# Optimization experiments

Hardware: AMD Instinct MI355X
Metric: run time of the kernel (lower is better)

Reference implementation:

```python
import jax, jax.numpy as jnp
import numpy as np

CLIPS_NUM = 4
OUTPUT_SIZE = 1000000  # outputSize: number of features in trainset (scales Z)
T = 0.07               # temperature
QUEUE_K = 131072       # queue size
D = 128                # inputSize (feature dim)
BS = 256               # batch_size * clips_num


def _l2norm(x):
    return x / jnp.linalg.norm(x, axis=-1, keepdims=True)


def setup_inputs() -> dict:
    key = jax.random.key(0)
    kq, kk, km = jax.random.split(key, 3)
    # MoCo-style L2-normalized features keep exp(sim/T) finite.
    q = _l2norm(jax.random.normal(kq, (BS, D), jnp.float32))
    k = _l2norm(jax.random.normal(kk, (BS, D), jnp.float32))
    memory = _l2norm(jax.random.normal(km, (QUEUE_K, D), jnp.float32))
    return {"q": q, "k": k, "memory": memory, "i": 0}


def _make_indices(bs, clips_num):
    """Static (numpy) replication of MemoryMoCo.prepare_indices."""
    batch_size = bs // clips_num
    # indices[v] = row indices of all clips of video v: [batch_size, clips_num]
    indices = np.arange(bs).reshape(clips_num, batch_size).T
    vid = np.arange(bs) % batch_size
    all_clips = vid[:, None] + np.arange(clips_num)[None, :] * batch_size  # [bs, clips_num]
    mask = all_clips != np.arange(bs)[:, None]
    pos_indices = all_clips[mask].reshape(bs, clips_num - 1)  # drop self
    return jnp.asarray(indices), jnp.asarray(pos_indices)


def reference(q, k, memory, i):
    bs, d = q.shape
    batch_size = bs // CLIPS_NUM
    indices, pos_indices = _make_indices(bs, CLIPS_NUM)

    k = jax.lax.stop_gradient(k)            # k = k.detach()
    mem = jax.lax.stop_gradient(memory)     # queue = memory.clone().detach()

    # l_pos: gather positives, per-row bmm with q, mean over positives -> [bs, 1]
    positives = k[pos_indices]              # [bs, clips_num-1, d]
    l_pos = jnp.mean(jnp.einsum('bpd,bd->bp', positives, q), axis=-1, keepdims=True)

    # l_neg: queue GEMM -> [bs, K]
    l_neg = q @ mem.T

    out = jnp.concatenate([l_pos, l_neg], axis=1)   # [bs, 1+K]
    out = jnp.exp(out / T)
    # First-call NCE normalization: Z = out.mean() * outputSize (Z is detached in torch)
    Z = jax.lax.stop_gradient(jnp.mean(out) * OUTPUT_SIZE)
    out = out / Z

    probs = jnp.mean(out[:, 0] / jnp.sum(out, axis=1))  # extract_probs

    # no_grad memory-bank update: scatter mean of each video's clip keys
    out_ids = jnp.arange(batch_size) % memory.shape[0]   # index=0, fmod queueSize
    k_mean = jnp.mean(k[indices], axis=1)                # [batch_size, d]
    new_memory = memory.at[out_ids].set(k_mean)

    return out, probs, new_memory
```

## Files before the change

### kernel.cpp

```cpp
#include <hip/hip_runtime.h>
#include <hip/hip_bf16.h>

constexpr int       DIM        = 128;
constexpr long long CN         = 131073;
constexpr long long OUT_ELEMS  = 256LL * 131073LL;
constexpr long long PROBS_OFF  = OUT_ELEMS;
constexpr long long MEMOUT_OFF = OUT_ELEMS + 1;
constexpr long long MEM_ELEMS  = 131072LL * 128LL;

constexpr float SCL = 20.60992915555662f;

constexpr int WS_INVZ  = 0;
constexpr int WS_ELPOS = 16;
constexpr int WS_KMEAN = 272;
constexpr int WS_ROWP  = 8464;
constexpr int WS_QB    = 16656;
constexpr int WS_MEMBF = 33040;

constexpr int PB_Q    = 8192;
constexpr int PB_KM   = 8208;
constexpr int PB_LPOS = 8240;
constexpr int PB_ZERO = 8304;
constexpr int PREP_BLOCKS = 8308;

typedef __attribute__((ext_vector_type(8))) short  short8v;
typedef __attribute__((ext_vector_type(4))) float  f32x4;

__device__ __forceinline__ unsigned short f2bf(float x) {
  unsigned u = __float_as_uint(x);
  u += 0x7fffu + ((u >> 16) & 1u);
  return (unsigned short)(u >> 16);
}

__device__ __forceinline__ short8v pack8(float4 a, float4 b) {
  short8v h;
  h[0] = (short)f2bf(a.x); h[1] = (short)f2bf(a.y);
  h[2] = (short)f2bf(a.z); h[3] = (short)f2bf(a.w);
  h[4] = (short)f2bf(b.x); h[5] = (short)f2bf(b.y);
  h[6] = (short)f2bf(b.z); h[7] = (short)f2bf(b.w);
  return h;
}

__global__ __launch_bounds__(256) void k_prep(const float* __restrict__ q,
                                              const float* __restrict__ k,
                                              const float* __restrict__ memv,
                                              float* __restrict__ ws) {
  const int b = blockIdx.x, t = threadIdx.x;
  if (b < PB_Q) {
    long long gid = (long long)b * 256 + t;
    const float4* src = (const float4*)memv;
    float4 a = src[2 * gid], c = src[2 * gid + 1];
    short8v* dst = (short8v*)((unsigned short*)(ws + WS_MEMBF) + gid * 8);
    *dst = pack8(a, c);
  } else if (b < PB_KM) {
    int gid = (b - PB_Q) * 256 + t;
    const float4* src = (const float4*)q;
    float4 a = src[2 * gid], c = src[2 * gid + 1];
    short8v* dst = (short8v*)((unsigned short*)(ws + WS_QB) + gid * 8);
    *dst = pack8(a, c);
  } else if (b < PB_LPOS) {
    int j = (b - PB_KM) * 256 + t;
    int v = j >> 7, d = j & 127;
    ws[WS_KMEAN + j] = 0.25f * (k[v*128+d] + k[(v+64)*128+d] +
                                k[(v+128)*128+d] + k[(v+192)*128+d]);
  } else if (b < PB_ZERO) {
    int row = (b - PB_LPOS) * 4 + (t >> 6);
    int lane = t & 63;
    int vid = row & 63;
    float2 qv = ((const float2*)(q + row * DIM))[lane];
    float2 kr = ((const float2*)(k + row * DIM))[lane];
    float s0 = -kr.x, s1 = -kr.y;
    #pragma unroll
    for (int c = 0; c < 4; ++c) {
      float2 kc = ((const float2*)(k + (vid + c * 64) * DIM))[lane];
      s0 += kc.x; s1 += kc.y;
    }
    float acc = qv.x * s0 + qv.y * s1;
    #pragma unroll
    for (int off = 1; off < 64; off <<= 1) acc += __shfl_xor(acc, off, 64);
    if (lane == 0) ws[WS_ELPOS + row] = exp2f(acc * (1.f / 3.f) * SCL);
  } else {
    int i = (b - PB_ZERO) * 2048 + t * 8;
    float4 z = {0.f, 0.f, 0.f, 0.f};
    *(float4*)(ws + WS_ROWP + i)     = z;
    *(float4*)(ws + WS_ROWP + i + 4) = z;
  }
}

template<int PASS, int NT, int GRID>
__global__ __launch_bounds__(256) void k_gemm(const unsigned short* __restrict__ membf,
                                              const unsigned short* __restrict__ qb,
                                              float* __restrict__ ws,
                                              float* __restrict__ out) {
  const int t = threadIdx.x, lane = t & 63, wave = t >> 6;
  const int g = lane >> 4, nlo = lane & 15;
  float invZ = 0.f;
  if (PASS == 1) invZ = ws[WS_INVZ];

  short8v af[4][4];
  #pragma unroll
  for (int ks = 0; ks < 4; ++ks)
    #pragma unroll
    for (int mf = 0; mf < 4; ++mf)
      af[ks][mf] = *(const short8v*)(qb + (wave*64 + mf*16 + nlo) * DIM + ks*32 + g*8);

  float sums[4][4];
  if (PASS == 0) {
    #pragma unroll
    for (int mf = 0; mf < 4; ++mf)
      #pragma unroll
      for (int r = 0; r < 4; ++r) sums[mf][r] = 0.f;
  }

  for (int it = 0; it < NT; ++it) {
    const int tile = blockIdx.x + it * GRID;
    const long long n0 = (long long)tile * 32;
    f32x4 acc[4][2];
    f32x4 zero = {0.f, 0.f, 0.f, 0.f};
    #pragma unroll
    for (int mf = 0; mf < 4; ++mf) { acc[mf][0] = zero; acc[mf][1] = zero; }

    #pragma unroll
    for (int ks = 0; ks < 4; ++ks) {
      short8v b0 = *(const short8v*)(membf + (n0 + nlo)      * DIM + ks*32 + g*8);
      short8v b1 = *(const short8v*)(membf + (n0 + 16 + nlo) * DIM + ks*32 + g*8);
      #pragma unroll
      for (int mf = 0; mf < 4; ++mf) {
        acc[mf][0] = __builtin_amdgcn_mfma_f32_16x16x32_bf16(af[ks][mf], b0, acc[mf][0], 0, 0, 0);
        acc[mf][1] = __builtin_amdgcn_mfma_f32_16x16x32_bf16(af[ks][mf], b1, acc[mf][1], 0, 0, 0);
      }
    }

    #pragma unroll
    for (int mf = 0; mf < 4; ++mf) {
      #pragma unroll
      for (int r = 0; r < 4; ++r) {
        float v0 = exp2f(acc[mf][0][r] * SCL);
        float v1 = exp2f(acc[mf][1][r] * SCL);
        if (PASS == 0) {
          sums[mf][r] += v0 + v1;
        } else {
          int row = wave*64 + mf*16 + g*4 + r;
          long long base = (long long)row * CN + 1 + n0;
          out[base + nlo]      = v0 * invZ;
          out[base + 16 + nlo] = v1 * invZ;
        }
      }
    }
  }

  if (PASS == 0) {
    float* rowp = ws + WS_ROWP + (blockIdx.x & 31) * 256;
    #pragma unroll
    for (int mf = 0; mf < 4; ++mf) {
      #pragma unroll
      for (int r = 0; r < 4; ++r) {
        float s = sums[mf][r];
        s += __shfl_xor(s, 1, 16);
        s += __shfl_xor(s, 2, 16);
        s += __shfl_xor(s, 4, 16);
        s += __shfl_xor(s, 8, 16);
        if (nlo == 0) atomicAdd(&rowp[wave*64 + mf*16 + g*4 + r], s);
      }
    }
  }
}

__global__ void k_fin(float* __restrict__ ws, float* __restrict__ out) {
  __shared__ float s_tot[256];
  __shared__ float s_pr[256];
  __shared__ float sh_invZ;
  int t = threadIdx.x;
  float s = ws[WS_ELPOS + t];
  float rs = s;
  for (int sl = 0; sl < 32; ++sl) rs += ws[WS_ROWP + sl * 256 + t];
  s_tot[t] = rs;
  s_pr[t] = s / rs;
  __syncthreads();
  for (int off = 128; off > 0; off >>= 1) {
    if (t < off) { s_tot[t] += s_tot[t + off]; s_pr[t] += s_pr[t + off]; }
    __syncthreads();
  }
  if (t == 0) {
    double Z = (double)s_tot[0] * (1000000.0 / (256.0 * 131073.0));
    float invZ = (float)(1.0 / Z);
    ws[WS_INVZ] = invZ;
    sh_invZ = invZ;
    out[PROBS_OFF] = s_pr[0] * (1.f / 256.f);
  }
  __syncthreads();
  out[(long long)t * CN] = s * sh_invZ;
}

__global__ void k_copy(const float* __restrict__ memv, const float* __restrict__ ws,
                       float* __restrict__ out) {
  float* dst = out + MEMOUT_OFF;
  const float* km = ws + WS_KMEAN;
  long long gid = blockIdx.x * 256LL + threadIdx.x;
  if (gid == 0) {
    dst[0] = km[0]; dst[1] = km[1]; dst[2] = km[2];
    dst[MEM_ELEMS - 1] = memv[MEM_ELEMS - 1];
  }
  const long long ng = (MEM_ELEMS - 4) / 4;
  long long stride = (long long)gridDim.x * 256LL;
  for (long long i = gid; i < ng; i += stride) {
    long long base = 3 + i * 4;
    float4 v;
    if (base + 4 <= 8192) {
      v.x = km[base]; v.y = km[base+1]; v.z = km[base+2]; v.w = km[base+3];
    } else if (base >= 8192) {
      v.x = memv[base]; v.y = memv[base+1]; v.z = memv[base+2]; v.w = memv[base+3];
    } else {
      float tmp[4];
      #pragma unroll
      for (int e = 0; e < 4; ++e) {
        long long idx = base + e;
        tmp[e] = (idx < 8192) ? km[idx] : memv[idx];
      }
      v.x = tmp[0]; v.y = tmp[1]; v.z = tmp[2]; v.w = tmp[3];
    }
    *(float4*)(dst + base) = v;
  }
}

extern "C" void kernel_launch(void* const* d_in, const int* in_sizes, int n_in,
                              void* d_out, int out_size, void* d_ws, size_t ws_size,
                              hipStream_t stream) {
  (void)in_sizes; (void)n_in; (void)out_size; (void)ws_size;
  const float* q    = (const float*)d_in[0];
  const float* k    = (const float*)d_in[1];
  const float* memv = (const float*)d_in[2];
  float* out = (float*)d_out;
  float* ws  = (float*)d_ws;
  const unsigned short* membf = (const unsigned short*)(ws + WS_MEMBF);
  const unsigned short* qb    = (const unsigned short*)(ws + WS_QB);

  hipLaunchKernelGGL(k_prep, dim3(PREP_BLOCKS), dim3(256), 0, stream, q, k, memv, ws);
  hipLaunchKernelGGL((k_gemm<0, 8, 512>),  dim3(512),  dim3(256), 0, stream, membf, qb, ws, out);
  hipLaunchKernelGGL(k_fin,  dim3(1),    dim3(256), 0, stream, ws, out);
  hipLaunchKernelGGL((k_gemm<1, 4, 1024>), dim3(1024), dim3(256), 0, stream, membf, qb, ws, out);
  hipLaunchKernelGGL(k_copy, dim3(2048), dim3(256), 0, stream, memv, ws, out);
}
```

Baseline: 399.8 us.

## Fuse bf16 conversion into first GEMM pass and restructure output pass

Drops the separate bf16 conversion of the memory bank and q from the prep kernel. The first GEMM pass now reads fp32 memory directly, packs it to bf16, and writes the packed copy for the second pass, while q is packed in registers. The second pass now uses contiguous per-block tile ranges with a swizzled block order, precomputed row offsets and a 512-block grid. The copy kernel is also simplified into aligned vector copies with the boundary elements handled separately. Together these remove one full pass over the 64MB memory bank, at the cost of redundant fp32 reads across waves in the fused pass.

```diff
diff --git a/kernel.cpp b/kernel.cpp
--- a/kernel.cpp
+++ b/kernel.cpp
@@ -14,17 +14,11 @@
 constexpr int WS_ELPOS = 16;
 constexpr int WS_KMEAN = 272;
 constexpr int WS_ROWP  = 8464;
-constexpr int WS_QB    = 16656;
-constexpr int WS_MEMBF = 33040;
-
-constexpr int PB_Q    = 8192;
-constexpr int PB_KM   = 8208;
-constexpr int PB_LPOS = 8240;
-constexpr int PB_ZERO = 8304;
-constexpr int PREP_BLOCKS = 8308;
+constexpr int WS_MEMBF = 16656;
 
 typedef __attribute__((ext_vector_type(8))) short  short8v;
 typedef __attribute__((ext_vector_type(4))) float  f32x4;
+typedef __attribute__((ext_vector_type(4), aligned(4))) float f32x4u;
 
 __device__ __forceinline__ unsigned short f2bf(float x) {
   unsigned u = __float_as_uint(x);
@@ -43,28 +37,15 @@
 
 __global__ __launch_bounds__(256) void k_prep(const float* __restrict__ q,
                                               const float* __restrict__ k,
-                                              const float* __restrict__ memv,
                                               float* __restrict__ ws) {
   const int b = blockIdx.x, t = threadIdx.x;
-  if (b < PB_Q) {
-    long long gid = (long long)b * 256 + t;
-    const float4* src = (const float4*)memv;
-    float4 a = src[2 * gid], c = src[2 * gid + 1];
-    short8v* dst = (short8v*)((unsigned short*)(ws + WS_MEMBF) + gid * 8);
-    *dst = pack8(a, c);
-  } else if (b < PB_KM) {
-    int gid = (b - PB_Q) * 256 + t;
-    const float4* src = (const float4*)q;
-    float4 a = src[2 * gid], c = src[2 * gid + 1];
-    short8v* dst = (short8v*)((unsigned short*)(ws + WS_QB) + gid * 8);
-    *dst = pack8(a, c);
-  } else if (b < PB_LPOS) {
-    int j = (b - PB_KM) * 256 + t;
+  if (b < 32) {
+    int j = b * 256 + t;
     int v = j >> 7, d = j & 127;
     ws[WS_KMEAN + j] = 0.25f * (k[v*128+d] + k[(v+64)*128+d] +
                                 k[(v+128)*128+d] + k[(v+192)*128+d]);
-  } else if (b < PB_ZERO) {
-    int row = (b - PB_LPOS) * 4 + (t >> 6);
+  } else if (b < 96) {
+    int row = (b - 32) * 4 + (t >> 6);
     int lane = t & 63;
     int vid = row & 63;
     float2 qv = ((const float2*)(q + row * DIM))[lane];
@@ -80,41 +61,38 @@
     for (int off = 1; off < 64; off <<= 1) acc += __shfl_xor(acc, off, 64);
     if (lane == 0) ws[WS_ELPOS + row] = exp2f(acc * (1.f / 3.f) * SCL);
   } else {
-    int i = (b - PB_ZERO) * 2048 + t * 8;
+    int i = (b - 96) * 2048 + t * 8;
     float4 z = {0.f, 0.f, 0.f, 0.f};
     *(float4*)(ws + WS_ROWP + i)     = z;
     *(float4*)(ws + WS_ROWP + i + 4) = z;
   }
 }
 
-template<int PASS, int NT, int GRID>
-__global__ __launch_bounds__(256) void k_gemm(const unsigned short* __restrict__ membf,
-                                              const unsigned short* __restrict__ qb,
-                                              float* __restrict__ ws,
-                                              float* __restrict__ out) {
+template<int NT>
+__global__ __launch_bounds__(256) void k_gemm0(const float* __restrict__ memv,
+                                               const float* __restrict__ q,
+                                               unsigned short* __restrict__ membf,
+                                               float* __restrict__ ws) {
   const int t = threadIdx.x, lane = t & 63, wave = t >> 6;
   const int g = lane >> 4, nlo = lane & 15;
-  float invZ = 0.f;
-  if (PASS == 1) invZ = ws[WS_INVZ];
 
   short8v af[4][4];
   #pragma unroll
   for (int ks = 0; ks < 4; ++ks)
     #pragma unroll
-    for (int mf = 0; mf < 4; ++mf)
-      af[ks][mf] = *(const short8v*)(qb + (wave*64 + mf*16 + nlo) * DIM + ks*32 + g*8);
+    for (int mf = 0; mf < 4; ++mf) {
+      const float4* src = (const float4*)(q + (wave*64 + mf*16 + nlo)*DIM + ks*32 + g*8);
+      af[ks][mf] = pack8(src[0], src[1]);
+    }
 
   float sums[4][4];
-  if (PASS == 0) {
-    #pragma unroll
-    for (int mf = 0; mf < 4; ++mf)
-      #pragma unroll
-      for (int r = 0; r < 4; ++r) sums[mf][r] = 0.f;
-  }
+  #pragma unroll
+  for (int mf = 0; mf < 4; ++mf)
+    #pragma unroll
+    for (int r = 0; r < 4; ++r) sums[mf][r] = 0.f;
 
   for (int it = 0; it < NT; ++it) {
-    const int tile = blockIdx.x + it * GRID;
-    const long long n0 = (long long)tile * 32;
+    const long long n0 = ((long long)blockIdx.x * NT + it) * 32;
     f32x4 acc[4][2];
     f32x4 zero = {0.f, 0.f, 0.f, 0.f};
     #pragma unroll
@@ -122,46 +100,37 @@
 
     #pragma unroll
     for (int ks = 0; ks < 4; ++ks) {
-      short8v b0 = *(const short8v*)(membf + (n0 + nlo)      * DIM + ks*32 + g*8);
-      short8v b1 = *(const short8v*)(membf + (n0 + 16 + nlo) * DIM + ks*32 + g*8);
-      #pragma unroll
-      for (int mf = 0; mf < 4; ++mf) {
-        acc[mf][0] = __builtin_amdgcn_mfma_f32_16x16x32_bf16(af[ks][mf], b0, acc[mf][0], 0, 0, 0);
-        acc[mf][1] = __builtin_amdgcn_mfma_f32_16x16x32_bf16(af[ks][mf], b1, acc[mf][1], 0, 0, 0);
+      #pragma unroll
+      for (int nf = 0; nf < 2; ++nf) {
+        const long long off = (n0 + nf*16 + nlo) * DIM + ks*32 + g*8;
+        const float4* src = (const float4*)(memv + off);
+        short8v bfr = pack8(src[0], src[1]);
+        if (wave == ks)
+          *(short8v*)(membf + off) = bfr;
+        #pragma unroll
+        for (int mf = 0; mf < 4; ++mf)
+          acc[mf][nf] = __builtin_amdgcn_mfma_f32_16x16x32_bf16(af[ks][mf], bfr, acc[mf][nf], 0, 0, 0);
       }
     }
 
     #pragma unroll
-    for (int mf = 0; mf < 4; ++mf) {
-      #pragma unroll
-      for (int r = 0; r < 4; ++r) {
-        float v0 = exp2f(acc[mf][0][r] * SCL);
-        float v1 = exp2f(acc[mf][1][r] * SCL);
-        if (PASS == 0) {
-          sums[mf][r] += v0 + v1;
-        } else {
-          int row = wave*64 + mf*16 + g*4 + r;
-          long long base = (long long)row * CN + 1 + n0;
-          out[base + nlo]      = v0 * invZ;
-          out[base + 16 + nlo] = v1 * invZ;
-        }
-      }
-    }
-  }
-
-  if (PASS == 0) {
-    float* rowp = ws + WS_ROWP + (blockIdx.x & 31) * 256;
-    #pragma unroll
-    for (int mf = 0; mf < 4; ++mf) {
-      #pragma unroll
-      for (int r = 0; r < 4; ++r) {
-        float s = sums[mf][r];
-        s += __shfl_xor(s, 1, 16);
-        s += __shfl_xor(s, 2, 16);
-        s += __shfl_xor(s, 4, 16);
-        s += __shfl_xor(s, 8, 16);
-        if (nlo == 0) atomicAdd(&rowp[wave*64 + mf*16 + g*4 + r], s);
-      }
+    for (int mf = 0; mf < 4; ++mf)
+      #pragma unroll
+      for (int r = 0; r < 4; ++r)
+        sums[mf][r] += exp2f(acc[mf][0][r] * SCL) + exp2f(acc[mf][1][r] * SCL);
+  }
+
+  float* rowp = ws + WS_ROWP + (blockIdx.x & 31) * 256;
+  #pragma unroll
+  for (int mf = 0; mf < 4; ++mf) {
+    #pragma unroll
+    for (int r = 0; r < 4; ++r) {
+      float s = sums[mf][r];
+      s += __shfl_xor(s, 1, 16);
+      s += __shfl_xor(s, 2, 16);
+      s += __shfl_xor(s, 4, 16);
+      s += __shfl_xor(s, 8, 16);
+      if (nlo == 0) atomicAdd(&rowp[wave*64 + mf*16 + g*4 + r], s);
     }
   }
 }
@@ -192,6 +161,63 @@
   out[(long long)t * CN] = s * sh_invZ;
 }
 
+template<int NT>
+__global__ __launch_bounds__(256) void k_gemm1(const unsigned short* __restrict__ membf,
+                                               const float* __restrict__ q,
+                                               const float* __restrict__ ws,
+                                               float* __restrict__ out) {
+  const int t = threadIdx.x, lane = t & 63, wave = t >> 6;
+  const int g = lane >> 4, nlo = lane & 15;
+  const float invZ = ws[WS_INVZ];
+
+  short8v af[4][4];
+  #pragma unroll
+  for (int ks = 0; ks < 4; ++ks)
+    #pragma unroll
+    for (int mf = 0; mf < 4; ++mf) {
+      const float4* src = (const float4*)(q + (wave*64 + mf*16 + nlo)*DIM + ks*32 + g*8);
+      af[ks][mf] = pack8(src[0], src[1]);
+    }
+
+  long long rowoff[4][4];
+  #pragma unroll
+  for (int mf = 0; mf < 4; ++mf)
+    #pragma unroll
+    for (int r = 0; r < 4; ++r)
+      rowoff[mf][r] = (long long)(wave*64 + mf*16 + g*4 + r) * CN + 1 + nlo;
+
+  const int logical = (blockIdx.x & 7) * 64 + (blockIdx.x >> 3);
+  const long long t0 = (long long)logical * NT;
+
+  for (int it = 0; it < NT; ++it) {
+    const long long n0 = (t0 + it) * 32;
+    f32x4 acc[4][2];
+    f32x4 zero = {0.f, 0.f, 0.f, 0.f};
+    #pragma unroll
+    for (int mf = 0; mf < 4; ++mf) { acc[mf][0] = zero; acc[mf][1] = zero; }
+
+    #pragma unroll
+    for (int ks = 0; ks < 4; ++ks) {
+      short8v b0 = *(const short8v*)(membf + (n0 + nlo)      * DIM + ks*32 + g*8);
+      short8v b1 = *(const short8v*)(membf + (n0 + 16 + nlo) * DIM + ks*32 + g*8);
+      #pragma unroll
+      for (int mf = 0; mf < 4; ++mf) {
+        acc[mf][0] = __builtin_amdgcn_mfma_f32_16x16x32_bf16(af[ks][mf], b0, acc[mf][0], 0, 0, 0);
+        acc[mf][1] = __builtin_amdgcn_mfma_f32_16x16x32_bf16(af[ks][mf], b1, acc[mf][1], 0, 0, 0);
+      }
+    }
+
+    #pragma unroll
+    for (int mf = 0; mf < 4; ++mf) {
+      #pragma unroll
+      for (int r = 0; r < 4; ++r) {
+        out[rowoff[mf][r] + n0]      = exp2f(acc[mf][0][r] * SCL) * invZ;
+        out[rowoff[mf][r] + n0 + 16] = exp2f(acc[mf][1][r] * SCL) * invZ;
+      }
+    }
+  }
+}
+
 __global__ void k_copy(const float* __restrict__ memv, const float* __restrict__ ws,
                        float* __restrict__ out) {
   float* dst = out + MEMOUT_OFF;
@@ -199,27 +225,21 @@
   long long gid = blockIdx.x * 256LL + threadIdx.x;
   if (gid == 0) {
     dst[0] = km[0]; dst[1] = km[1]; dst[2] = km[2];
+    dst[8191] = km[8191];
+    dst[8192] = memv[8192]; dst[8193] = memv[8193]; dst[8194] = memv[8194];
     dst[MEM_ELEMS - 1] = memv[MEM_ELEMS - 1];
   }
-  const long long ng = (MEM_ELEMS - 4) / 4;
-  long long stride = (long long)gridDim.x * 256LL;
-  for (long long i = gid; i < ng; i += stride) {
-    long long base = 3 + i * 4;
-    float4 v;
-    if (base + 4 <= 8192) {
-      v.x = km[base]; v.y = km[base+1]; v.z = km[base+2]; v.w = km[base+3];
-    } else if (base >= 8192) {
-      v.x = memv[base]; v.y = memv[base+1]; v.z = memv[base+2]; v.w = memv[base+3];
-    } else {
-      float tmp[4];
-      #pragma unroll
-      for (int e = 0; e < 4; ++e) {
-        long long idx = base + e;
-        tmp[e] = (idx < 8192) ? km[idx] : memv[idx];
-      }
-      v.x = tmp[0]; v.y = tmp[1]; v.z = tmp[2]; v.w = tmp[3];
-    }
-    *(float4*)(dst + base) = v;
+  if (gid < 2047) {
+    long long base = 3 + gid * 4;
+    f32x4u v = *(const f32x4u*)(km + base);
+    *(f32x4u*)(dst + base) = v;
+  }
+  const long long NGB = (MEM_ELEMS - 1 - 8195) / 4;
+  const long long stride = (long long)gridDim.x * 256LL;
+  for (long long j = gid; j < NGB; j += stride) {
+    long long base = 8195 + j * 4;
+    f32x4u v = *(const f32x4u*)(memv + base);
+    *(f32x4u*)(dst + base) = v;
   }
 }
 
@@ -232,12 +252,11 @@
   const float* memv = (const float*)d_in[2];
   float* out = (float*)d_out;
   float* ws  = (float*)d_ws;
-  const unsigned short* membf = (const unsigned short*)(ws + WS_MEMBF);
-  const unsigned short* qb    = (const unsigned short*)(ws + WS_QB);
-
-  hipLaunchKernelGGL(k_prep, dim3(PREP_BLOCKS), dim3(256), 0, stream, q, k, memv, ws);
-  hipLaunchKernelGGL((k_gemm<0, 8, 512>),  dim3(512),  dim3(256), 0, stream, membf, qb, ws, out);
-  hipLaunchKernelGGL(k_fin,  dim3(1),    dim3(256), 0, stream, ws, out);
-  hipLaunchKernelGGL((k_gemm<1, 4, 1024>), dim3(1024), dim3(256), 0, stream, membf, qb, ws, out);
+  unsigned short* membf = (unsigned short*)(ws + WS_MEMBF);
+
+  hipLaunchKernelGGL(k_prep, dim3(100), dim3(256), 0, stream, q, k, ws);
+  hipLaunchKernelGGL((k_gemm0<8>), dim3(512), dim3(256), 0, stream, memv, q, membf, ws);
+  hipLaunchKernelGGL(k_fin,  dim3(1),   dim3(256), 0, stream, ws, out);
+  hipLaunchKernelGGL((k_gemm1<8>), dim3(512), dim3(256), 0, stream, membf, q, ws, out);
   hipLaunchKernelGGL(k_copy, dim3(2048), dim3(256), 0, stream, memv, ws, out);
 }
```

Result: slower. 409.1 us (+2.3%).
